# Performance work log

Hardware: AMD Instinct MI355X
Metric: run time of the kernel (lower is better)

## Reference

```python
import jax, jax.numpy as jnp
import numpy as np

N, D, H = 65536, 512, 256  # batch, input_dim, hidden_dim
BN_EPS = 1e-5
EPS = 1e-15


def setup_inputs() -> dict:
    key = jax.random.key(0)
    ks = jax.random.split(key, 10)
    rn = lambda k, shape, sc: jax.random.normal(k, shape, dtype=jnp.float32) * sc
    return {
        "x1": rn(ks[0], (N, D), 1.0),
        "x2": rn(ks[1], (N, D), 1.0),
        "W1": rn(ks[2], (D, H), 0.04),
        "b1": jnp.zeros((H,), jnp.float32),
        "gamma": jnp.ones((H,), jnp.float32),
        "beta_bn": jnp.zeros((H,), jnp.float32),
        "W2": rn(ks[3], (H, H // 2), 0.06),
        "b2": jnp.zeros((H // 2,), jnp.float32),
        "W3": rn(ks[4], (H // 2 * 3, 64), 0.05),
        "b3": jnp.zeros((64,), jnp.float32),
        "W4": rn(ks[5], (64, 1), 0.12),
        "b4": jnp.zeros((1,), jnp.float32),
        "alpha": jnp.array([0.65], jnp.float32),
        "beta": jnp.array([0.25], jnp.float32),
    }


def _proj(x, W1, b1, gamma, beta_bn, W2, b2):
    h = x @ W1 + b1                       # [N, 256]
    mean = jnp.mean(h, axis=0)
    var = jnp.var(h, axis=0)              # biased, matches BN training normalization
    h = gamma * (h - mean) * jax.lax.rsqrt(var + BN_EPS) + beta_bn
    h = jax.nn.relu(h)
    return jax.nn.relu(h @ W2 + b2)       # [N, 128]


def reference(x1, x2, W1, b1, gamma, beta_bn, W2, b2, W3, b3, W4, b4, alpha, beta):
    h1 = _proj(x1, W1, b1, gamma, beta_bn, W2, b2)
    h2 = _proj(x2, W1, b1, gamma, beta_bn, W2, b2)
    # diag of normalized similarity matrix == row-wise cosine similarity
    dot = jnp.sum(h1 * h2, axis=1)
    inv1 = 1.0 / jnp.maximum(jnp.sqrt(jnp.sum(h1 * h1, axis=1)), EPS)
    inv2 = 1.0 / jnp.maximum(jnp.sqrt(jnp.sum(h2 * h2, axis=1)), EPS)
    s_math = jnp.clip(dot * inv1 * inv2, 0.0, 1.0)
    combined = jnp.concatenate([h1 * h2, jnp.abs(h1 - h2), h1 + h2], axis=1)  # [N, 384]
    s_learn = (jax.nn.relu(combined @ W3 + b3) @ W4 + b4).reshape(-1)          # [N]
    final = alpha * s_math + beta * jax.nn.sigmoid(s_learn)
    return jnp.clip(final, 0.0, 1.0)
```

## Files before the change

kernel.cpp:

```cpp
#include <hip/hip_runtime.h>
#include <hip/hip_bf16.h>
#include <math.h>

#define NROWS 65536
#define DIN   512
#define H1    256
#define H2    128
#define K3DIM 384
#define O3    64

typedef short  short8  __attribute__((ext_vector_type(8)));
typedef float  f32x4   __attribute__((ext_vector_type(4)));
typedef unsigned short u16x4 __attribute__((ext_vector_type(4)));

__device__ __forceinline__ unsigned short f2bf(float f) {
    union { float f; unsigned int i; } v; v.f = f;
    unsigned int r = (v.i + 0x7fffu + ((v.i >> 16) & 1u)) >> 16;
    return (unsigned short)r;
}
__device__ __forceinline__ float bf2f(unsigned short u) {
    union { unsigned int i; float f; } v; v.i = ((unsigned int)u) << 16;
    return v.f;
}

__global__ void prep_kernel(const float* __restrict__ W1, const float* __restrict__ W2,
                            const float* __restrict__ W3,
                            unsigned short* __restrict__ w1t, unsigned short* __restrict__ w2t,
                            unsigned short* __restrict__ w3t) {
    int idx = blockIdx.x * 256 + threadIdx.x;
    if (idx < DIN * H1) {
        int c = idx >> 9, r = idx & 511;
        w1t[idx] = f2bf(W1[r * H1 + c]);
    } else if (idx < DIN * H1 + H1 * H2) {
        int i2 = idx - DIN * H1;
        int c = i2 >> 8, r = i2 & 255;
        w2t[i2] = f2bf(W2[r * H2 + c]);
    } else if (idx < DIN * H1 + H1 * H2 + K3DIM * O3) {
        int i3 = idx - DIN * H1 - H1 * H2;
        int c = i3 / K3DIM, r = i3 - c * K3DIM;
        w3t[i3] = f2bf(W3[r * O3 + c]);
    }
}

#define LDA 40

__global__ __launch_bounds__(256, 3)
void gemm1_kernel(const float* __restrict__ x1, const float* __restrict__ x2,
                  const unsigned short* __restrict__ w1t, const float* __restrict__ b1,
                  unsigned short* __restrict__ h_out, float* __restrict__ stats) {
    __shared__ __align__(16) unsigned short Al[128 * LDA];
    __shared__ __align__(16) unsigned short Bl[128 * LDA];
    const int t  = threadIdx.x;
    const int n0 = blockIdx.x * 128;
    const int m0 = blockIdx.y * 128;
    const float* xp = (m0 < NROWS) ? x1 : x2;
    const int inp = (m0 < NROWS) ? 0 : 1;
    const int r0 = m0 & (NROWS - 1);

    const int wave = t >> 6, lane = t & 63;
    const int wm = wave >> 1, wn = wave & 1;
    const int m = lane & 15, q = lane >> 4;

    const int ar = t >> 1, ah = t & 1;
    const float* abase = xp + (size_t)(r0 + ar) * DIN + ah * 16;
    const unsigned short* bbase = w1t + (size_t)(n0 + ar) * DIN + ah * 16;

    f32x4 acc[4][4] = {};
    float4 pa[4];
    float4 pb[2];

#pragma unroll
    for (int i = 0; i < 4; ++i) pa[i] = *reinterpret_cast<const float4*>(abase + i * 4);
    pb[0] = *reinterpret_cast<const float4*>(bbase);
    pb[1] = *reinterpret_cast<const float4*>(bbase + 8);

    for (int k0 = 0; k0 < DIN; k0 += 32) {
        __syncthreads();
        {
            unsigned short ob[16] __attribute__((aligned(16)));
#pragma unroll
            for (int i = 0; i < 4; ++i) {
                ob[4 * i + 0] = f2bf(pa[i].x); ob[4 * i + 1] = f2bf(pa[i].y);
                ob[4 * i + 2] = f2bf(pa[i].z); ob[4 * i + 3] = f2bf(pa[i].w);
            }
            *reinterpret_cast<float4*>(&Al[ar * LDA + ah * 16])     = *reinterpret_cast<float4*>(ob);
            *reinterpret_cast<float4*>(&Al[ar * LDA + ah * 16 + 8]) = *reinterpret_cast<float4*>(ob + 8);
            *reinterpret_cast<float4*>(&Bl[ar * LDA + ah * 16])     = pb[0];
            *reinterpret_cast<float4*>(&Bl[ar * LDA + ah * 16 + 8]) = pb[1];
        }
        __syncthreads();
        if (k0 + 32 < DIN) {
#pragma unroll
            for (int i = 0; i < 4; ++i) pa[i] = *reinterpret_cast<const float4*>(abase + k0 + 32 + i * 4);
            pb[0] = *reinterpret_cast<const float4*>(bbase + k0 + 32);
            pb[1] = *reinterpret_cast<const float4*>(bbase + k0 + 32 + 8);
        }
        short8 af[4], bfr[4];
#pragma unroll
        for (int mi = 0; mi < 4; ++mi)
            af[mi] = *reinterpret_cast<const short8*>(&Al[(wm * 64 + mi * 16 + m) * LDA + q * 8]);
#pragma unroll
        for (int ni = 0; ni < 4; ++ni)
            bfr[ni] = *reinterpret_cast<const short8*>(&Bl[(wn * 64 + ni * 16 + m) * LDA + q * 8]);
#pragma unroll
        for (int mi = 0; mi < 4; ++mi)
#pragma unroll
            for (int ni = 0; ni < 4; ++ni)
                acc[mi][ni] = __builtin_amdgcn_mfma_f32_16x16x32_bf16(af[mi], bfr[ni], acc[mi][ni], 0, 0, 0);
    }

    float s[4] = {0.f, 0.f, 0.f, 0.f}, ss[4] = {0.f, 0.f, 0.f, 0.f};
#pragma unroll
    for (int ni = 0; ni < 4; ++ni) {
        int col = n0 + wn * 64 + ni * 16 + m;
        float bias = b1[col];
#pragma unroll
        for (int mi = 0; mi < 4; ++mi) {
#pragma unroll
            for (int r = 0; r < 4; ++r) {
                int row = m0 + wm * 64 + mi * 16 + q * 4 + r;
                float v = acc[mi][ni][r] + bias;
                h_out[(size_t)row * H1 + col] = f2bf(v);
                s[ni] += v; ss[ni] += v * v;
            }
        }
    }
#pragma unroll
    for (int ni = 0; ni < 4; ++ni) {
        s[ni]  += __shfl_xor(s[ni], 16);  s[ni]  += __shfl_xor(s[ni], 32);
        ss[ni] += __shfl_xor(ss[ni], 16); ss[ni] += __shfl_xor(ss[ni], 32);
    }
    if (q == 0) {
#pragma unroll
        for (int ni = 0; ni < 4; ++ni) {
            int col = n0 + wn * 64 + ni * 16 + m;
            atomicAdd(&stats[inp * 2 * H1 + col], s[ni]);
            atomicAdd(&stats[inp * 2 * H1 + H1 + col], ss[ni]);
        }
    }
}

__global__ void bnparams_kernel(const float* __restrict__ stats, const float* __restrict__ gamma,
                                const float* __restrict__ beta_bn, float* __restrict__ ab) {
    int t = threadIdx.x;
    int inp = t >> 8, c = t & 255;
    float mean = stats[(inp * 2 + 0) * H1 + c] * (1.0f / NROWS);
    float ex2  = stats[(inp * 2 + 1) * H1 + c] * (1.0f / NROWS);
    float var  = ex2 - mean * mean;
    float a = gamma[c] * rsqrtf(var + 1e-5f);
    ab[(inp * 2 + 0) * H1 + c] = a;
    ab[(inp * 2 + 1) * H1 + c] = beta_bn[c] - a * mean;
}

__global__ __launch_bounds__(256, 3)
void gemm2_kernel(const unsigned short* __restrict__ h, const unsigned short* __restrict__ w2t,
                  const float* __restrict__ b2, const float* __restrict__ ab,
                  unsigned short* __restrict__ z) {
    __shared__ __align__(16) unsigned short Al[128 * LDA];
    __shared__ __align__(16) unsigned short Bl[128 * LDA];
    __shared__ float sc[H1], sh[H1];
    const int t  = threadIdx.x;
    const int m0 = blockIdx.x * 128;
    const int inp = m0 >> 16;
    sc[t & 255] = ab[inp * 2 * H1 + (t & 255)];
    sh[t & 255] = ab[inp * 2 * H1 + H1 + (t & 255)];

    const int wave = t >> 6, lane = t & 63;
    const int wm = wave >> 1, wn = wave & 1;
    const int m = lane & 15, q = lane >> 4;

    const int ar = t >> 1, ah = t & 1;
    const unsigned short* abase = h + (size_t)(m0 + ar) * H1 + ah * 16;
    const unsigned short* bbase = w2t + (size_t)ar * H1 + ah * 16;

    f32x4 acc[4][4] = {};
    float4 pa[2], pb[2];
    pa[0] = *reinterpret_cast<const float4*>(abase);
    pa[1] = *reinterpret_cast<const float4*>(abase + 8);
    pb[0] = *reinterpret_cast<const float4*>(bbase);
    pb[1] = *reinterpret_cast<const float4*>(bbase + 8);

    for (int k0 = 0; k0 < H1; k0 += 32) {
        __syncthreads();
        {
            unsigned short vs[16] __attribute__((aligned(16)));
            unsigned short ob[16] __attribute__((aligned(16)));
            *reinterpret_cast<float4*>(vs)     = pa[0];
            *reinterpret_cast<float4*>(vs + 8) = pa[1];
#pragma unroll
            for (int j = 0; j < 16; ++j) {
                int k = k0 + ah * 16 + j;
                float v = sc[k] * bf2f(vs[j]) + sh[k];
                ob[j] = f2bf(fmaxf(v, 0.f));
            }
            *reinterpret_cast<float4*>(&Al[ar * LDA + ah * 16])     = *reinterpret_cast<float4*>(ob);
            *reinterpret_cast<float4*>(&Al[ar * LDA + ah * 16 + 8]) = *reinterpret_cast<float4*>(ob + 8);
            *reinterpret_cast<float4*>(&Bl[ar * LDA + ah * 16])     = pb[0];
            *reinterpret_cast<float4*>(&Bl[ar * LDA + ah * 16 + 8]) = pb[1];
        }
        __syncthreads();
        if (k0 + 32 < H1) {
            pa[0] = *reinterpret_cast<const float4*>(abase + k0 + 32);
            pa[1] = *reinterpret_cast<const float4*>(abase + k0 + 32 + 8);
            pb[0] = *reinterpret_cast<const float4*>(bbase + k0 + 32);
            pb[1] = *reinterpret_cast<const float4*>(bbase + k0 + 32 + 8);
        }
        short8 af[4], bfr[4];
#pragma unroll
        for (int mi = 0; mi < 4; ++mi)
            af[mi] = *reinterpret_cast<const short8*>(&Al[(wm * 64 + mi * 16 + m) * LDA + q * 8]);
#pragma unroll
        for (int ni = 0; ni < 4; ++ni)
            bfr[ni] = *reinterpret_cast<const short8*>(&Bl[(wn * 64 + ni * 16 + m) * LDA + q * 8]);
#pragma unroll
        for (int mi = 0; mi < 4; ++mi)
#pragma unroll
            for (int ni = 0; ni < 4; ++ni)
                acc[mi][ni] = __builtin_amdgcn_mfma_f32_16x16x32_bf16(af[mi], bfr[ni], acc[mi][ni], 0, 0, 0);
    }
#pragma unroll
    for (int mi = 0; mi < 4; ++mi)
#pragma unroll
        for (int ni = 0; ni < 4; ++ni) {
            int col = wn * 64 + ni * 16 + m;
            float bias = b2[col];
#pragma unroll
            for (int r = 0; r < 4; ++r) {
                int row = m0 + wm * 64 + mi * 16 + q * 4 + r;
                z[(size_t)row * H2 + col] = f2bf(fmaxf(acc[mi][ni][r] + bias, 0.f));
            }
        }
}

#define LDW3 392

__global__ __launch_bounds__(512)
void head_kernel(const unsigned short* __restrict__ z, const unsigned short* __restrict__ w3t,
                 const float* __restrict__ b3, const float* __restrict__ w4,
                 const float* __restrict__ b4, const float* __restrict__ alpha,
                 const float* __restrict__ beta, float* __restrict__ out) {
    __shared__ __align__(16) unsigned short W3l[64 * LDW3];
    __shared__ float b3s[64], w4s[64];
    __shared__ float smath[128], slearn[128];

    const int t  = threadIdx.x;
    const int r0 = blockIdx.x * 128;

#pragma unroll
    for (int i = 0; i < 3; ++i) {
        int c = t + i * 512;
        int n = c / 24, kc = c - n * 24;
        const float4* src = reinterpret_cast<const float4*>(w3t + n * K3DIM + kc * 16);
        float4 v0 = src[0], v1 = src[1];
        *reinterpret_cast<float4*>(&W3l[n * LDW3 + kc * 16])     = v0;
        *reinterpret_cast<float4*>(&W3l[n * LDW3 + kc * 16 + 8]) = v1;
    }
    if (t < 64) { b3s[t] = b3[t]; w4s[t] = w4[t]; }
    __syncthreads();

    const int wave = t >> 6, lane = t & 63;
    const int m = lane & 15, q = lane >> 4;
    const int wr = wave * 16;
    const int row = r0 + wr + m;

    short8 z1c[4], z2c[4];
#pragma unroll
    for (int c = 0; c < 4; ++c) {
        z1c[c] = *reinterpret_cast<const short8*>(z + (size_t)row * H2 + c * 32 + q * 8);
        z2c[c] = *reinterpret_cast<const short8*>(z + (size_t)(NROWS + row) * H2 + c * 32 + q * 8);
    }

    float d = 0.f, s1 = 0.f, s2 = 0.f;
    f32x4 acc[4] = {};
#pragma unroll
    for (int kb = 0; kb < 12; ++kb) {
        int seg = kb >> 2, c = kb & 3;
        short8 af;
#pragma unroll
        for (int j = 0; j < 8; ++j) {
            float v1 = bf2f((unsigned short)z1c[c][j]);
            float v2 = bf2f((unsigned short)z2c[c][j]);
            float v;
            if (seg == 0) { v = v1 * v2; d += v; s1 += v1 * v1; s2 += v2 * v2; }
            else if (seg == 1) v = fabsf(v1 - v2);
            else v = v1 + v2;
            af[j] = (short)f2bf(v);
        }
#pragma unroll
        for (int ni = 0; ni < 4; ++ni) {
            short8 bfr = *reinterpret_cast<const short8*>(&W3l[(ni * 16 + m) * LDW3 + kb * 32 + q * 8]);
            acc[ni] = __builtin_amdgcn_mfma_f32_16x16x32_bf16(af, bfr, acc[ni], 0, 0, 0);
        }
    }
    d  += __shfl_xor(d, 16);  d  += __shfl_xor(d, 32);
    s1 += __shfl_xor(s1, 16); s1 += __shfl_xor(s1, 32);
    s2 += __shfl_xor(s2, 16); s2 += __shfl_xor(s2, 32);
    if (q == 0) {
        float inv1 = 1.f / fmaxf(sqrtf(s1), 1e-15f);
        float inv2 = 1.f / fmaxf(sqrtf(s2), 1e-15f);
        smath[wr + m] = fminf(fmaxf(d * inv1 * inv2, 0.f), 1.f);
    }

    float partial[4] = {0.f, 0.f, 0.f, 0.f};
#pragma unroll
    for (int ni = 0; ni < 4; ++ni) {
        int col = ni * 16 + m;
        float bias = b3s[col], w4v = w4s[col];
#pragma unroll
        for (int rg = 0; rg < 4; ++rg) {
            float v = fmaxf(acc[ni][rg] + bias, 0.f);
            partial[rg] += v * w4v;
        }
    }
#pragma unroll
    for (int rg = 0; rg < 4; ++rg) {
        float p = partial[rg];
        p += __shfl_xor(p, 1); p += __shfl_xor(p, 2);
        p += __shfl_xor(p, 4); p += __shfl_xor(p, 8);
        if (m == 0) slearn[wr + q * 4 + rg] = p + b4[0];
    }
    __syncthreads();
    if (t < 128) {
        float sl = slearn[t];
        float sig = 1.f / (1.f + expf(-sl));
        float f = alpha[0] * smath[t] + beta[0] * sig;
        out[r0 + t] = fminf(fmaxf(f, 0.f), 1.f);
    }
}

extern "C" void kernel_launch(void* const* d_in, const int* in_sizes, int n_in,
                              void* d_out, int out_size, void* d_ws, size_t ws_size,
                              hipStream_t stream) {
    (void)in_sizes; (void)n_in; (void)out_size; (void)ws_size;
    const float* x1      = (const float*)d_in[0];
    const float* x2      = (const float*)d_in[1];
    const float* W1      = (const float*)d_in[2];
    const float* b1      = (const float*)d_in[3];
    const float* gamma   = (const float*)d_in[4];
    const float* beta_bn = (const float*)d_in[5];
    const float* W2      = (const float*)d_in[6];
    const float* b2      = (const float*)d_in[7];
    const float* W3      = (const float*)d_in[8];
    const float* b3      = (const float*)d_in[9];
    const float* W4      = (const float*)d_in[10];
    const float* b4      = (const float*)d_in[11];
    const float* alpha   = (const float*)d_in[12];
    const float* beta    = (const float*)d_in[13];
    float* out = (float*)d_out;

    char* ws = (char*)d_ws;
    unsigned short* h   = (unsigned short*)(ws);
    unsigned short* w1t = (unsigned short*)(ws + 67108864);
    unsigned short* w2t = (unsigned short*)(ws + 67371008);
    unsigned short* w3t = (unsigned short*)(ws + 67436544);
    float*          stats = (float*)(ws + 67485696);
    float*          ab    = (float*)(ws + 67489792);
    unsigned short* z   = (unsigned short*)(ws + 67493888);

    (void)hipMemsetAsync(stats, 0, 4096, stream);
    prep_kernel<<<(DIN * H1 + H1 * H2 + K3DIM * O3 + 255) / 256, 256, 0, stream>>>(W1, W2, W3, w1t, w2t, w3t);
    gemm1_kernel<<<dim3(2, 1024), 256, 0, stream>>>(x1, x2, w1t, b1, h, stats);
    bnparams_kernel<<<1, 512, 0, stream>>>(stats, gamma, beta_bn, ab);
    gemm2_kernel<<<1024, 256, 0, stream>>>(h, w2t, b2, ab, z);
    head_kernel<<<512, 512, 0, stream>>>(z, w3t, b3, W4, b4, alpha, beta, out);
}
```

Before: 454.4 us.

## Replace BN stat atomics with partial-sum buffer and retune GEMM/head kernels

Gemm1 now writes per-block column sums and sums of squares into a partial buffer instead of issuing atomics. A new two-block reduce kernel folds those partials and computes the BN scale and shift, which also removes the memset. Gemm1 drops its register prefetch of the next K-tile, loads and converts x straight into shared memory, and relaxes its occupancy hint. Gemm2 gets a higher occupancy hint and reordered stores, and the head kernel moves to 256-thread blocks over 64 rows each. The risks are losing the load/compute overlap in the dominant GEMM and a serial reduction over 1024 slots per column.

After: 426.6 us. 1.07x faster.

```diff
diff --git a/kernel.cpp b/kernel.cpp
--- a/kernel.cpp
+++ b/kernel.cpp
@@ -44,57 +44,42 @@
 
 #define LDA 40
 
-__global__ __launch_bounds__(256, 3)
+__global__ __launch_bounds__(256, 2)
 void gemm1_kernel(const float* __restrict__ x1, const float* __restrict__ x2,
                   const unsigned short* __restrict__ w1t, const float* __restrict__ b1,
-                  unsigned short* __restrict__ h_out, float* __restrict__ stats) {
+                  unsigned short* __restrict__ h_out, float* __restrict__ P) {
     __shared__ __align__(16) unsigned short Al[128 * LDA];
     __shared__ __align__(16) unsigned short Bl[128 * LDA];
     const int t  = threadIdx.x;
     const int n0 = blockIdx.x * 128;
     const int m0 = blockIdx.y * 128;
     const float* xp = (m0 < NROWS) ? x1 : x2;
-    const int inp = (m0 < NROWS) ? 0 : 1;
     const int r0 = m0 & (NROWS - 1);
 
     const int wave = t >> 6, lane = t & 63;
     const int wm = wave >> 1, wn = wave & 1;
     const int m = lane & 15, q = lane >> 4;
 
-    const int ar = t >> 1, ah = t & 1;
-    const float* abase = xp + (size_t)(r0 + ar) * DIN + ah * 16;
-    const unsigned short* bbase = w1t + (size_t)(n0 + ar) * DIN + ah * 16;
-
     f32x4 acc[4][4] = {};
-    float4 pa[4];
-    float4 pb[2];
-
-#pragma unroll
-    for (int i = 0; i < 4; ++i) pa[i] = *reinterpret_cast<const float4*>(abase + i * 4);
-    pb[0] = *reinterpret_cast<const float4*>(bbase);
-    pb[1] = *reinterpret_cast<const float4*>(bbase + 8);
 
     for (int k0 = 0; k0 < DIN; k0 += 32) {
         __syncthreads();
+#pragma unroll
+        for (int i = 0; i < 4; ++i) {
+            int u = t + i * 256;
+            int r = u >> 3, kq = u & 7;
+            const float4 v = *reinterpret_cast<const float4*>(xp + (size_t)(r0 + r) * DIN + k0 + kq * 4);
+            u16x4 b; b.x = f2bf(v.x); b.y = f2bf(v.y); b.z = f2bf(v.z); b.w = f2bf(v.w);
+            *reinterpret_cast<u16x4*>(&Al[r * LDA + kq * 4]) = b;
+        }
         {
-            unsigned short ob[16] __attribute__((aligned(16)));
-#pragma unroll
-            for (int i = 0; i < 4; ++i) {
-                ob[4 * i + 0] = f2bf(pa[i].x); ob[4 * i + 1] = f2bf(pa[i].y);
-                ob[4 * i + 2] = f2bf(pa[i].z); ob[4 * i + 3] = f2bf(pa[i].w);
-            }
-            *reinterpret_cast<float4*>(&Al[ar * LDA + ah * 16])     = *reinterpret_cast<float4*>(ob);
-            *reinterpret_cast<float4*>(&Al[ar * LDA + ah * 16 + 8]) = *reinterpret_cast<float4*>(ob + 8);
-            *reinterpret_cast<float4*>(&Bl[ar * LDA + ah * 16])     = pb[0];
-            *reinterpret_cast<float4*>(&Bl[ar * LDA + ah * 16 + 8]) = pb[1];
+            int n = t >> 1, kh = t & 1;
+            const float4* src = reinterpret_cast<const float4*>(w1t + (size_t)(n0 + n) * DIN + k0 + kh * 16);
+            float4 v0 = src[0], v1 = src[1];
+            *reinterpret_cast<float4*>(&Bl[n * LDA + kh * 16])     = v0;
+            *reinterpret_cast<float4*>(&Bl[n * LDA + kh * 16 + 8]) = v1;
         }
         __syncthreads();
-        if (k0 + 32 < DIN) {
-#pragma unroll
-            for (int i = 0; i < 4; ++i) pa[i] = *reinterpret_cast<const float4*>(abase + k0 + 32 + i * 4);
-            pb[0] = *reinterpret_cast<const float4*>(bbase + k0 + 32);
-            pb[1] = *reinterpret_cast<const float4*>(bbase + k0 + 32 + 8);
-        }
         short8 af[4], bfr[4];
 #pragma unroll
         for (int mi = 0; mi < 4; ++mi)
@@ -111,11 +96,11 @@
 
     float s[4] = {0.f, 0.f, 0.f, 0.f}, ss[4] = {0.f, 0.f, 0.f, 0.f};
 #pragma unroll
-    for (int ni = 0; ni < 4; ++ni) {
-        int col = n0 + wn * 64 + ni * 16 + m;
-        float bias = b1[col];
-#pragma unroll
-        for (int mi = 0; mi < 4; ++mi) {
+    for (int mi = 0; mi < 4; ++mi)
+#pragma unroll
+        for (int ni = 0; ni < 4; ++ni) {
+            int col = n0 + wn * 64 + ni * 16 + m;
+            float bias = b1[col];
 #pragma unroll
             for (int r = 0; r < 4; ++r) {
                 int row = m0 + wm * 64 + mi * 16 + q * 4 + r;
@@ -124,35 +109,49 @@
                 s[ni] += v; ss[ni] += v * v;
             }
         }
-    }
 #pragma unroll
     for (int ni = 0; ni < 4; ++ni) {
         s[ni]  += __shfl_xor(s[ni], 16);  s[ni]  += __shfl_xor(s[ni], 32);
         ss[ni] += __shfl_xor(ss[ni], 16); ss[ni] += __shfl_xor(ss[ni], 32);
     }
     if (q == 0) {
+        const size_t mslot = (size_t)blockIdx.y * 2 + wm;
 #pragma unroll
         for (int ni = 0; ni < 4; ++ni) {
             int col = n0 + wn * 64 + ni * 16 + m;
-            atomicAdd(&stats[inp * 2 * H1 + col], s[ni]);
-            atomicAdd(&stats[inp * 2 * H1 + H1 + col], ss[ni]);
-        }
-    }
-}
-
-__global__ void bnparams_kernel(const float* __restrict__ stats, const float* __restrict__ gamma,
-                                const float* __restrict__ beta_bn, float* __restrict__ ab) {
-    int t = threadIdx.x;
-    int inp = t >> 8, c = t & 255;
-    float mean = stats[(inp * 2 + 0) * H1 + c] * (1.0f / NROWS);
-    float ex2  = stats[(inp * 2 + 1) * H1 + c] * (1.0f / NROWS);
-    float var  = ex2 - mean * mean;
-    float a = gamma[c] * rsqrtf(var + 1e-5f);
-    ab[(inp * 2 + 0) * H1 + c] = a;
-    ab[(inp * 2 + 1) * H1 + c] = beta_bn[c] - a * mean;
-}
-
-__global__ __launch_bounds__(256, 3)
+            P[mslot * 256 + col]                 = s[ni];
+            P[(size_t)524288 + mslot * 256 + col] = ss[ni];
+        }
+    }
+}
+
+__global__ __launch_bounds__(512)
+void reduce_bn_kernel(const float* __restrict__ P, const float* __restrict__ gamma,
+                      const float* __restrict__ beta_bn, float* __restrict__ ab) {
+    __shared__ float Ssum[256], SSsum[256];
+    const int inp = blockIdx.x;
+    const int t = threadIdx.x;
+    const int arr = t >> 8, col = t & 255;
+    const float* base = P + (size_t)arr * 524288 + (size_t)inp * 1024 * 256 + col;
+    float a0 = 0.f, a1 = 0.f, a2 = 0.f, a3 = 0.f;
+    for (int ms = 0; ms < 1024; ms += 4) {
+        a0 += base[(ms + 0) * 256]; a1 += base[(ms + 1) * 256];
+        a2 += base[(ms + 2) * 256]; a3 += base[(ms + 3) * 256];
+    }
+    float tot = (a0 + a1) + (a2 + a3);
+    if (arr == 0) Ssum[col] = tot; else SSsum[col] = tot;
+    __syncthreads();
+    if (t < 256) {
+        float mean = Ssum[t] * (1.0f / NROWS);
+        float ex2  = SSsum[t] * (1.0f / NROWS);
+        float var  = ex2 - mean * mean;
+        float a = gamma[t] * rsqrtf(var + 1e-5f);
+        ab[inp * 2 * H1 + t]      = a;
+        ab[inp * 2 * H1 + H1 + t] = beta_bn[t] - a * mean;
+    }
+}
+
+__global__ __launch_bounds__(256, 4)
 void gemm2_kernel(const unsigned short* __restrict__ h, const unsigned short* __restrict__ w2t,
                   const float* __restrict__ b2, const float* __restrict__ ab,
                   unsigned short* __restrict__ z) {
@@ -218,37 +217,40 @@
             for (int ni = 0; ni < 4; ++ni)
                 acc[mi][ni] = __builtin_amdgcn_mfma_f32_16x16x32_bf16(af[mi], bfr[ni], acc[mi][ni], 0, 0, 0);
     }
-#pragma unroll
-    for (int mi = 0; mi < 4; ++mi)
-#pragma unroll
-        for (int ni = 0; ni < 4; ++ni) {
-            int col = wn * 64 + ni * 16 + m;
-            float bias = b2[col];
-#pragma unroll
-            for (int r = 0; r < 4; ++r) {
-                int row = m0 + wm * 64 + mi * 16 + q * 4 + r;
-                z[(size_t)row * H2 + col] = f2bf(fmaxf(acc[mi][ni][r] + bias, 0.f));
+    float bias[4];
+#pragma unroll
+    for (int ni = 0; ni < 4; ++ni) bias[ni] = b2[wn * 64 + ni * 16 + m];
+#pragma unroll
+    for (int mi = 0; mi < 4; ++mi) {
+#pragma unroll
+        for (int r = 0; r < 4; ++r) {
+            int row = m0 + wm * 64 + mi * 16 + q * 4 + r;
+#pragma unroll
+            for (int ni = 0; ni < 4; ++ni) {
+                int col = wn * 64 + ni * 16 + m;
+                z[(size_t)row * H2 + col] = f2bf(fmaxf(acc[mi][ni][r] + bias[ni], 0.f));
             }
         }
+    }
 }
 
 #define LDW3 392
 
-__global__ __launch_bounds__(512)
+__global__ __launch_bounds__(256)
 void head_kernel(const unsigned short* __restrict__ z, const unsigned short* __restrict__ w3t,
                  const float* __restrict__ b3, const float* __restrict__ w4,
                  const float* __restrict__ b4, const float* __restrict__ alpha,
                  const float* __restrict__ beta, float* __restrict__ out) {
     __shared__ __align__(16) unsigned short W3l[64 * LDW3];
     __shared__ float b3s[64], w4s[64];
-    __shared__ float smath[128], slearn[128];
+    __shared__ float smath[64], slearn[64];
 
     const int t  = threadIdx.x;
-    const int r0 = blockIdx.x * 128;
-
-#pragma unroll
-    for (int i = 0; i < 3; ++i) {
-        int c = t + i * 512;
+    const int r0 = blockIdx.x * 64;
+
+#pragma unroll
+    for (int i = 0; i < 6; ++i) {
+        int c = t + i * 256;
         int n = c / 24, kc = c - n * 24;
         const float4* src = reinterpret_cast<const float4*>(w3t + n * K3DIM + kc * 16);
         float4 v0 = src[0], v1 = src[1];
@@ -320,7 +322,7 @@
         if (m == 0) slearn[wr + q * 4 + rg] = p + b4[0];
     }
     __syncthreads();
-    if (t < 128) {
+    if (t < 64) {
         float sl = slearn[t];
         float sig = 1.f / (1.f + expf(-sl));
         float f = alpha[0] * smath[t] + beta[0] * sig;
@@ -353,14 +355,13 @@
     unsigned short* w1t = (unsigned short*)(ws + 67108864);
     unsigned short* w2t = (unsigned short*)(ws + 67371008);
     unsigned short* w3t = (unsigned short*)(ws + 67436544);
-    float*          stats = (float*)(ws + 67485696);
-    float*          ab    = (float*)(ws + 67489792);
-    unsigned short* z   = (unsigned short*)(ws + 67493888);
-
-    (void)hipMemsetAsync(stats, 0, 4096, stream);
+    float*          ab  = (float*)(ws + 67485696);
+    unsigned short* z   = (unsigned short*)(ws + 67489792);
+    float*          P   = (float*)(ws + 67489792);
+
     prep_kernel<<<(DIN * H1 + H1 * H2 + K3DIM * O3 + 255) / 256, 256, 0, stream>>>(W1, W2, W3, w1t, w2t, w3t);
-    gemm1_kernel<<<dim3(2, 1024), 256, 0, stream>>>(x1, x2, w1t, b1, h, stats);
-    bnparams_kernel<<<1, 512, 0, stream>>>(stats, gamma, beta_bn, ab);
+    gemm1_kernel<<<dim3(2, 1024), 256, 0, stream>>>(x1, x2, w1t, b1, h, P);
+    reduce_bn_kernel<<<2, 512, 0, stream>>>(P, gamma, beta_bn, ab);
     gemm2_kernel<<<1024, 256, 0, stream>>>(h, w2t, b2, ab, z);
-    head_kernel<<<512, 512, 0, stream>>>(z, w3t, b3, W4, b4, alpha, beta, out);
-}
+    head_kernel<<<1024, 256, 0, stream>>>(z, w3t, b3, W4, b4, alpha, beta, out);
+}
```
